# Kernel tuning notes

Hardware: AMD Instinct MI355X
Metric: run time of the kernel (lower is better)

## Reference

```python
import jax, jax.numpy as jnp
import numpy as np

N_NODES = 100000
N_EDGES = 6400000


def setup_inputs() -> dict:
    key = jax.random.key(0)
    ks = jax.random.split(key, 20)
    g = lambda i, shape, fan_in: jax.random.normal(ks[i], shape, dtype=jnp.float32) / np.sqrt(fan_in)
    inp = {
        "x": jax.random.normal(ks[0], (N_NODES, 32), dtype=jnp.float32),
        "edge_index": jax.random.randint(ks[1], (2, N_EDGES), 0, N_NODES, dtype=jnp.int64),
        # encoder: Linear(32,240) -> ReLU -> Linear(240,24) -> ReLU
        "enc_w1": g(2, (32, 240), 32), "enc_b1": jnp.zeros((240,), jnp.float32),
        "enc_w2": g(3, (240, 24), 240), "enc_b2": jnp.zeros((24,), jnp.float32),
        # lin_r (applied to root, no bias) -- PyG defaults
        "sage1_wl": g(4, (24, 24), 24), "sage1_bl": jnp.zeros((24,), jnp.float32), "sage1_wr": g(5, (24, 24), 24),
        "sage2_wl": g(6, (24, 24), 24), "sage2_bl": jnp.zeros((24,), jnp.float32), "sage2_wr": g(7, (24, 24), 24),
        "sage3_wl": g(8, (24, 24), 24), "sage3_bl": jnp.zeros((24,), jnp.float32), "sage3_wr": g(9, (24, 24), 24),
        # decoder: Linear(24,120) -> ReLU -> Linear(120,12)
        "dec_w1": g(10, (24, 120), 24), "dec_b1": jnp.zeros((120,), jnp.float32),
        "dec_w2": g(11, (120, 12), 120), "dec_b2": jnp.zeros((12,), jnp.float32),
    }
    return inp


def _sage_conv(x, src, dst, wl, bl, wr, n_nodes):
    # mean aggregation: gather source features, scatter-sum at targets, divide by degree
    msg = x[src]                                                   # [E, H]
    agg = jax.ops.segment_sum(msg, dst, num_segments=n_nodes)      # [N, H]
    deg = jax.ops.segment_sum(jnp.ones((src.shape[0],), x.dtype), dst, num_segments=n_nodes)
    mean = agg / jnp.maximum(deg, 1.0)[:, None]
    return mean @ wl + bl + x @ wr


def reference(x, edge_index, enc_w1, enc_b1, enc_w2, enc_b2,
              sage1_wl, sage1_bl, sage1_wr,
              sage2_wl, sage2_bl, sage2_wr,
              sage3_wl, sage3_bl, sage3_wr,
              dec_w1, dec_b1, dec_w2, dec_b2):
    n = x.shape[0]
    src, dst = edge_index[0], edge_index[1]
    # encoder
    h = jax.nn.relu(x @ enc_w1 + enc_b1)
    h = jax.nn.relu(h @ enc_w2 + enc_b2)
    # GNN: SAGEConv -> ReLU -> SAGEConv -> ReLU -> SAGEConv
    h = jax.nn.relu(_sage_conv(h, src, dst, sage1_wl, sage1_bl, sage1_wr, n))
    h = jax.nn.relu(_sage_conv(h, src, dst, sage2_wl, sage2_bl, sage2_wr, n))
    h = _sage_conv(h, src, dst, sage3_wl, sage3_bl, sage3_wr, n)
    # decoder
    h = jax.nn.relu(h @ dec_w1 + dec_b1)
    return h @ dec_w2 + dec_b2
```

## Files before the change

kernel.cpp:

```cpp
#include <hip/hip_runtime.h>
#include <hip/hip_bf16.h>

#define N_NODES 100000
#define N_EDGES 6400000
#define BROW 24
#define PROW 8
#define BUCKET_SIZE 256
#define N_BUCKETS ((N_NODES + BUCKET_SIZE - 1) / BUCKET_SIZE)
#define BUCKET_CAP 17408
#define STAGE_CAP 22528
#define SENT 0xFFFFFFFFu
#define STAGE_BLOCKS 512
#define CHUNK ((N_EDGES + STAGE_BLOCKS - 1) / STAGE_BLOCKS)

typedef float floatx2 __attribute__((ext_vector_type(2)));

__device__ __forceinline__ unsigned short f2bf(float f) {
    unsigned u = __float_as_uint(f);
    unsigned r = (u + 0x7fffu + ((u >> 16) & 1u)) >> 16;
    return (unsigned short)r;
}

__device__ __forceinline__ unsigned pack_fp8_4(float a, float b, float c, float d) {
    int w = __builtin_amdgcn_cvt_pk_fp8_f32(a, b, 0, false);
    w = __builtin_amdgcn_cvt_pk_fp8_f32(c, d, w, true);
    return (unsigned)w;
}

#define DEC4(w, arr, j) { \
    floatx2 lo_ = __builtin_amdgcn_cvt_pk_f32_fp8((int)(w), false); \
    floatx2 hi_ = __builtin_amdgcn_cvt_pk_f32_fp8((int)(w), true);  \
    arr[j] += lo_.x; arr[(j)+1] += lo_.y; arr[(j)+2] += hi_.x; arr[(j)+3] += hi_.y; }

#define SET2(u, arr, j) { arr[j] = __uint_as_float((u) << 16); arr[(j)+1] = __uint_as_float((u) & 0xffff0000u); }

__global__ __launch_bounds__(256) void k_transpose_w1(
    const float* __restrict__ w1, float* __restrict__ w1t)
{
    int tid = blockIdx.x * blockDim.x + threadIdx.x;
    if (tid < 32 * 240) {
        int k = tid >> 5, i = tid & 31;
        w1t[tid] = w1[i * 240 + k];
    }
}

__global__ __launch_bounds__(256) void k_enc_part(
    const float* __restrict__ x,
    const float* __restrict__ w1t, const float* __restrict__ b1,
    const float* __restrict__ w2,
    float* __restrict__ part)
{
    int nb = blockIdx.x >> 1;
    int chunk = blockIdx.x & 1;
    int n = nb * 256 + threadIdx.x;
    if (n >= N_NODES) return;

    float xr[32];
    const float4* xv = (const float4*)(x + (size_t)n * 32);
#pragma unroll
    for (int i = 0; i < 8; ++i) {
        float4 t = xv[i];
        xr[4*i+0] = t.x; xr[4*i+1] = t.y; xr[4*i+2] = t.z; xr[4*i+3] = t.w;
    }
    float acc[24];
#pragma unroll
    for (int j = 0; j < 24; ++j) acc[j] = 0.f;

    int k0 = chunk * 120;
    for (int k = k0; k < k0 + 120; ++k) {
        const float4* wr = (const float4*)(w1t + k * 32);
        float t = b1[k];
#pragma unroll
        for (int q = 0; q < 8; ++q) {
            float4 w = wr[q];
            t += xr[4*q+0] * w.x + xr[4*q+1] * w.y + xr[4*q+2] * w.z + xr[4*q+3] * w.w;
        }
        t = fmaxf(t, 0.f);
        const float* w2r = w2 + k * 24;
#pragma unroll
        for (int j = 0; j < 24; ++j) acc[j] += t * w2r[j];
    }
    float4* op = (float4*)(part + ((size_t)chunk * N_NODES + n) * 24);
#pragma unroll
    for (int c = 0; c < 6; ++c)
        op[c] = make_float4(acc[4*c], acc[4*c+1], acc[4*c+2], acc[4*c+3]);
}

__global__ __launch_bounds__(256) void k_enc_fin(
    const float* __restrict__ part, const float* __restrict__ b2,
    unsigned short* __restrict__ hb)
{
    int n = blockIdx.x * blockDim.x + threadIdx.x;
    if (n >= N_NODES) return;
    const float4* p0 = (const float4*)(part + (size_t)n * 24);
    const float4* p1 = (const float4*)(part + ((size_t)N_NODES + n) * 24);
    float acc[24];
#pragma unroll
    for (int c = 0; c < 6; ++c) {
        float4 a = p0[c], b = p1[c];
        acc[4*c+0] = a.x + b.x; acc[4*c+1] = a.y + b.y;
        acc[4*c+2] = a.z + b.z; acc[4*c+3] = a.w + b.w;
    }
    unsigned wb[12];
#pragma unroll
    for (int j = 0; j < 24; ++j) {
        float v = fmaxf(acc[j] + b2[j], 0.f);
        if (j & 1) wb[j >> 1] |= (unsigned)f2bf(v) << 16;
        else       wb[j >> 1]  = (unsigned)f2bf(v);
    }
    uint4* ob = (uint4*)(hb + (size_t)n * BROW);
#pragma unroll
    for (int q = 0; q < 3; ++q)
        ob[q] = make_uint4(wb[4*q], wb[4*q+1], wb[4*q+2], wb[4*q+3]);
}

__global__ __launch_bounds__(256) void k_stage1(
    const int* __restrict__ src, const int* __restrict__ dst,
    int* __restrict__ cursor, unsigned* __restrict__ stage)
{
    __shared__ int cnt[N_BUCKETS];
    __shared__ int bse[N_BUCKETS];
    __shared__ int lof[N_BUCKETS];
    __shared__ int cur[N_BUCKETS];
    __shared__ int ps[512];
    __shared__ unsigned sbuf[CHUNK];
    int t = threadIdx.x;
    int e0 = blockIdx.x * CHUNK;
    int e1 = min(e0 + CHUNK, N_EDGES);

    for (int i = t; i < N_BUCKETS; i += 256) cnt[i] = 0;
    __syncthreads();
    for (int e = e0 + t; e < e1; e += 256)
        atomicAdd(&cnt[dst[e] >> 8], 1);
    __syncthreads();
    for (int i = t; i < N_BUCKETS; i += 256) {
        int c = cnt[i];
        int c16 = (c + 15) & ~15;
        bse[i] = c16 ? atomicAdd(&cursor[i * 16], c16) : 0;
        cur[i] = 0;
    }
    ps[t]       = (t < N_BUCKETS) ? cnt[t] : 0;
    ps[t + 256] = (t + 256 < N_BUCKETS) ? cnt[t + 256] : 0;
    __syncthreads();
    for (int off = 1; off < 512; off <<= 1) {
        int a  = (t >= off) ? ps[t - off] : 0;
        int b2 = (t + 256 >= off) ? ps[t + 256 - off] : 0;
        __syncthreads();
        ps[t] += a;
        ps[t + 256] += b2;
        __syncthreads();
    }
    for (int i = t; i < N_BUCKETS; i += 256) lof[i] = ps[i] - cnt[i];
    __syncthreads();
    for (int e = e0 + t; e < e1; e += 256) {
        int d = dst[e];
        int s = src[e];
        int b = d >> 8;
        int pos = atomicAdd(&cur[b], 1);
        sbuf[lof[b] + pos] = ((unsigned)(d & 255) << 17) | (unsigned)s;
    }
    __syncthreads();
    int wid = t >> 6, lane = t & 63;
    for (int b = wid; b < N_BUCKETS; b += 4) {
        int c = cnt[b];
        int c16 = (c + 15) & ~15;
        unsigned* gp = stage + (size_t)b * STAGE_CAP + bse[b];
        const unsigned* lp = sbuf + lof[b];
        for (int j = lane; j < c16; j += 64)
            gp[j] = (j < c) ? lp[j] : SENT;
    }
}

__global__ __launch_bounds__(256) void k_fillcsr(
    const unsigned* __restrict__ stage, const int* __restrict__ cursor,
    int* __restrict__ csr, int* __restrict__ deg,
    float* __restrict__ recip, int* __restrict__ row_ptr)
{
    int b = blockIdx.x, t = threadIdx.x;
    __shared__ int dl[BUCKET_SIZE];
    __shared__ int s[BUCKET_SIZE];
    __shared__ int fcur[BUCKET_SIZE];
    int ne = cursor[b * 16];
    const unsigned* sp = stage + (size_t)b * STAGE_CAP;

    dl[t] = 0;
    __syncthreads();
    for (int i = t; i < ne; i += 256) {
        unsigned v = sp[i];
        if (v != SENT) atomicAdd(&dl[v >> 17], 1);
    }
    __syncthreads();
    int d = dl[t];
    s[t] = d;
    __syncthreads();
    for (int off = 1; off < 256; off <<= 1) {
        int v = (t >= off) ? s[t - off] : 0;
        __syncthreads();
        s[t] += v;
        __syncthreads();
    }
    int excl = s[t] - d;
    fcur[t] = excl;
    int n = b * BUCKET_SIZE + t;
    if (n < N_NODES) {
        deg[n] = d;
        recip[n] = 1.0f / (float)max(d, 1);
        row_ptr[n] = b * BUCKET_CAP + excl;
    }
    __syncthreads();
    int* cb = csr + (size_t)b * BUCKET_CAP;
    for (int i = t; i < ne; i += 256) {
        unsigned v = sp[i];
        if (v == SENT) continue;
        int slot = atomicAdd(&fcur[v >> 17], 1);
        cb[slot] = (int)(v & 0x1FFFFu);
    }
}

__global__ __launch_bounds__(256) void k_xform(
    const unsigned short* __restrict__ hin,
    const float* __restrict__ wl, const float* __restrict__ wr,
    unsigned* __restrict__ Ptab, float* __restrict__ Qtab)
{
    int n = blockIdx.x * blockDim.x + threadIdx.x;
    if (n >= N_NODES) return;
    float h[24];
    {
        const uint4* hp = (const uint4*)(hin + n * BROW);
        uint4 A = hp[0], B = hp[1], C = hp[2];
        SET2(A.x, h, 0)  SET2(A.y, h, 2)  SET2(A.z, h, 4)  SET2(A.w, h, 6)
        SET2(B.x, h, 8)  SET2(B.y, h,10)  SET2(B.z, h,12)  SET2(B.w, h,14)
        SET2(C.x, h,16)  SET2(C.y, h,18)  SET2(C.z, h,20)  SET2(C.w, h,22)
    }
    float p[24], q[24];
#pragma unroll
    for (int j = 0; j < 24; ++j) { p[j] = 0.f; q[j] = 0.f; }
#pragma unroll
    for (int k = 0; k < 24; ++k) {
        float hk = h[k];
#pragma unroll
        for (int j = 0; j < 24; ++j) {
            p[j] += hk * wl[k * 24 + j];
            q[j] += hk * wr[k * 24 + j];
        }
    }
    unsigned w8[6];
#pragma unroll
    for (int c = 0; c < 6; ++c)
        w8[c] = pack_fp8_4(p[4*c], p[4*c+1], p[4*c+2], p[4*c+3]);
    uint4* ob = (uint4*)(Ptab + (size_t)n * PROW);
    ob[0] = make_uint4(w8[0], w8[1], w8[2], w8[3]);
    ob[1] = make_uint4(w8[4], w8[5], 0u, 0u);
    float4* qb = (float4*)(Qtab + n * 24);
#pragma unroll
    for (int c = 0; c < 6; ++c)
        qb[c] = make_float4(q[4*c], q[4*c+1], q[4*c+2], q[4*c+3]);
}

template <bool RELU>
__global__ __launch_bounds__(256, 4) void k_agg(
    const unsigned* __restrict__ Ptab, const float* __restrict__ Qtab,
    const int* __restrict__ row_ptr, const int* __restrict__ deg,
    const float* __restrict__ recip, const int* __restrict__ csr,
    const float* __restrict__ bl,
    unsigned short* __restrict__ houtb)
{
    int gt = blockIdx.x * blockDim.x + threadIdx.x;
    int n = gt >> 3, g = gt & 7;
    if (n >= N_NODES) return;
    int start = row_ptr[n];
    int cnt = deg[n];

    float acc[24];
#pragma unroll
    for (int j = 0; j < 24; ++j) acc[j] = 0.f;

    for (int i = g; i < cnt; i += 8) {
        int s = __builtin_nontemporal_load(&csr[start + i]);
        const uint4* rp = (const uint4*)(Ptab + (size_t)s * PROW);
        uint4 A = rp[0];
        uint2 B = ((const uint2*)rp)[2];
        DEC4(A.x, acc, 0)  DEC4(A.y, acc, 4)  DEC4(A.z, acc, 8)
        DEC4(A.w, acc,12)  DEC4(B.x, acc,16)  DEC4(B.y, acc,20)
    }
#pragma unroll
    for (int m = 1; m <= 4; m <<= 1)
#pragma unroll
        for (int j = 0; j < 24; ++j) acc[j] += __shfl_xor(acc[j], m, 64);

    if (g < 3) {
        float rc = recip[n];
        const float4* qb = (const float4*)(Qtab + n * 24 + g * 8);
        float4 q0 = qb[0], q1 = qb[1];
        float qv[8] = {q0.x, q0.y, q0.z, q0.w, q1.x, q1.y, q1.z, q1.w};
        unsigned wb[4];
#pragma unroll
        for (int jj = 0; jj < 8; ++jj) {
            int j = g * 8 + jj;
            float v = acc[j] * rc + qv[jj] + bl[j];
            if (RELU) v = fmaxf(v, 0.f);
            if (jj & 1) wb[jj >> 1] |= (unsigned)f2bf(v) << 16;
            else        wb[jj >> 1]  = (unsigned)f2bf(v);
        }
        ((uint4*)(houtb + n * BROW))[g] = make_uint4(wb[0], wb[1], wb[2], wb[3]);
    }
}

__global__ __launch_bounds__(256, 4) void k_agg3(
    const unsigned* __restrict__ Ptab, const float* __restrict__ Qtab,
    const int* __restrict__ row_ptr, const int* __restrict__ deg,
    const float* __restrict__ recip, const int* __restrict__ csr,
    const float* __restrict__ bl,
    float* __restrict__ o3)
{
    int gt = blockIdx.x * blockDim.x + threadIdx.x;
    int n = gt >> 3, g = gt & 7;
    if (n >= N_NODES) return;
    int start = row_ptr[n];
    int cnt = deg[n];

    float acc[24];
#pragma unroll
    for (int j = 0; j < 24; ++j) acc[j] = 0.f;

    for (int i = g; i < cnt; i += 8) {
        int s = __builtin_nontemporal_load(&csr[start + i]);
        const uint4* rp = (const uint4*)(Ptab + (size_t)s * PROW);
        uint4 A = rp[0];
        uint2 B = ((const uint2*)rp)[2];
        DEC4(A.x, acc, 0)  DEC4(A.y, acc, 4)  DEC4(A.z, acc, 8)
        DEC4(A.w, acc,12)  DEC4(B.x, acc,16)  DEC4(B.y, acc,20)
    }
#pragma unroll
    for (int m = 1; m <= 4; m <<= 1)
#pragma unroll
        for (int j = 0; j < 24; ++j) acc[j] += __shfl_xor(acc[j], m, 64);

    if (g < 3) {
        float rc = recip[n];
        const float4* qb = (const float4*)(Qtab + n * 24 + g * 8);
        float4 q0 = qb[0], q1 = qb[1];
        float qv[8] = {q0.x, q0.y, q0.z, q0.w, q1.x, q1.y, q1.z, q1.w};
        float ov[8];
#pragma unroll
        for (int jj = 0; jj < 8; ++jj)
            ov[jj] = acc[g * 8 + jj] * rc + qv[jj] + bl[g * 8 + jj];
        float4* op = (float4*)(o3 + n * 24 + g * 8);
        op[0] = make_float4(ov[0], ov[1], ov[2], ov[3]);
        op[1] = make_float4(ov[4], ov[5], ov[6], ov[7]);
    }
}

__global__ __launch_bounds__(256) void k_decoder(
    const float* __restrict__ o3,
    const float* __restrict__ w1, const float* __restrict__ b1,
    const float* __restrict__ w2, const float* __restrict__ b2,
    float* __restrict__ out)
{
    int n = blockIdx.x * blockDim.x + threadIdx.x;
    if (n >= N_NODES) return;
    float h[24];
    const float4* hv = (const float4*)(o3 + (size_t)n * 24);
#pragma unroll
    for (int q = 0; q < 6; ++q) {
        float4 v = hv[q];
        h[4*q+0] = v.x; h[4*q+1] = v.y; h[4*q+2] = v.z; h[4*q+3] = v.w;
    }
    float acc[12];
#pragma unroll
    for (int j = 0; j < 12; ++j) acc[j] = b2[j];
    for (int k = 0; k < 120; ++k) {
        float t = b1[k];
#pragma unroll
        for (int i = 0; i < 24; ++i) t += h[i] * w1[i * 120 + k];
        t = fmaxf(t, 0.f);
#pragma unroll
        for (int j = 0; j < 12; ++j) acc[j] += t * w2[k * 12 + j];
    }
    float* o = out + (size_t)n * 12;
#pragma unroll
    for (int j = 0; j < 12; ++j) o[j] = acc[j];
}

static inline size_t align_up(size_t v, size_t a) { return (v + a - 1) & ~(a - 1); }

extern "C" void kernel_launch(void* const* d_in, const int* in_sizes, int n_in,
                              void* d_out, int out_size, void* d_ws, size_t ws_size,
                              hipStream_t stream)
{
    (void)in_sizes; (void)n_in; (void)out_size; (void)ws_size;

    const float* x    = (const float*)d_in[0];
    const int*  edge  = (const int*)d_in[1];
    const int*  esrc  = edge;
    const int*  edst  = edge + N_EDGES;
    const float* enc_w1 = (const float*)d_in[2];
    const float* enc_b1 = (const float*)d_in[3];
    const float* enc_w2 = (const float*)d_in[4];
    const float* enc_b2 = (const float*)d_in[5];
    const float* s1_wl = (const float*)d_in[6];
    const float* s1_bl = (const float*)d_in[7];
    const float* s1_wr = (const float*)d_in[8];
    const float* s2_wl = (const float*)d_in[9];
    const float* s2_bl = (const float*)d_in[10];
    const float* s2_wr = (const float*)d_in[11];
    const float* s3_wl = (const float*)d_in[12];
    const float* s3_bl = (const float*)d_in[13];
    const float* s3_wr = (const float*)d_in[14];
    const float* dec_w1 = (const float*)d_in[15];
    const float* dec_b1 = (const float*)d_in[16];
    const float* dec_w2 = (const float*)d_in[17];
    const float* dec_b2 = (const float*)d_in[18];
    float* out = (float*)d_out;

    char* base = (char*)d_ws;
    size_t off = 0;
    auto carve = [&](size_t bytes) { size_t o = off; off = align_up(off + bytes, 256); return (void*)(base + o); };
    char* stage_region = (char*)carve((size_t)N_BUCKETS * STAGE_CAP * sizeof(unsigned));
    unsigned* stage      = (unsigned*)stage_region;
    float* part          = (float*)stage_region;
    unsigned* Ptab       = (unsigned*)stage_region;
    float* Qtab          = (float*)(stage_region + 3200000);
    float* o3            = (float*)(stage_region + 12800000);
    int*   csr     = (int*)  carve((size_t)N_BUCKETS * BUCKET_CAP * sizeof(int));
    unsigned short* h0b = (unsigned short*)carve((size_t)N_NODES * BROW * sizeof(unsigned short));
    unsigned short* h1b = (unsigned short*)carve((size_t)N_NODES * BROW * sizeof(unsigned short));
    int*   deg     = (int*)  carve((size_t)N_NODES * sizeof(int));
    float* recip   = (float*)carve((size_t)N_NODES * sizeof(float));
    int*   row_ptr = (int*)  carve((size_t)N_NODES * sizeof(int));
    int*   cursor  = (int*)  carve((size_t)N_BUCKETS * 16 * sizeof(int));
    float* w1t     = (float*)carve((size_t)240 * 32 * sizeof(float));

    const int NB_N = (N_NODES + 255) / 256;
    const int NB8  = (N_NODES * 8 + 255) / 256;

    hipMemsetAsync(cursor, 0, (size_t)N_BUCKETS * 16 * sizeof(int), stream);
    k_stage1 <<<STAGE_BLOCKS, 256, 0, stream>>>(esrc, edst, cursor, stage);
    k_fillcsr<<<N_BUCKETS,   256, 0, stream>>>(stage, cursor, csr, deg, recip, row_ptr);

    k_transpose_w1<<<30, 256, 0, stream>>>(enc_w1, w1t);
    k_enc_part<<<NB_N * 2, 256, 0, stream>>>(x, w1t, enc_b1, enc_w2, part);
    k_enc_fin <<<NB_N,     256, 0, stream>>>(part, enc_b2, h0b);

    k_xform<<<NB_N, 256, 0, stream>>>(h0b, s1_wl, s1_wr, Ptab, Qtab);
    k_agg<true><<<NB8, 256, 0, stream>>>(Ptab, Qtab, row_ptr, deg, recip, csr, s1_bl, h1b);
    k_xform<<<NB_N, 256, 0, stream>>>(h1b, s2_wl, s2_wr, Ptab, Qtab);
    k_agg<true><<<NB8, 256, 0, stream>>>(Ptab, Qtab, row_ptr, deg, recip, csr, s2_bl, h0b);
    k_xform<<<NB_N, 256, 0, stream>>>(h0b, s3_wl, s3_wr, Ptab, Qtab);
    k_agg3<<<NB8, 256, 0, stream>>>(Ptab, Qtab, row_ptr, deg, recip, csr, s3_bl, o3);
    k_decoder<<<NB_N, 256, 0, stream>>>(o3, dec_w1, dec_b1, dec_w2, dec_b2, out);
}
```

Measured before the change: 527.5 us.

## Merge CSR fill with encoder into one launch and fuse encoder finish into xform

The CSR fill blocks and the encoder partial blocks now run in a single heterogeneous launch, so the graph-build work and the dense encoder can overlap on the device. The encoder partial sums are written as bf16 into the h0b/h1b buffers instead of fp32 into the stage region, which avoids overwriting stage before the fill reads it and halves the partial-sum traffic. The separate encoder-finish kernel is folded into the first xform, which now sums the two partials, adds the bias and applies ReLU before the SAGE transform. In exchange the partial sums are rounded to bf16 before they are added, which costs some precision, and the fused launch mixes block types with different resource needs.

Measured after the change: 484.5 us. -8.2%, faster.

```diff
diff --git a/kernel.cpp b/kernel.cpp
--- a/kernel.cpp
+++ b/kernel.cpp
@@ -33,6 +33,7 @@
     arr[j] += lo_.x; arr[(j)+1] += lo_.y; arr[(j)+2] += hi_.x; arr[(j)+3] += hi_.y; }
 
 #define SET2(u, arr, j) { arr[j] = __uint_as_float((u) << 16); arr[(j)+1] = __uint_as_float((u) & 0xffff0000u); }
+#define ADD2(u, arr, j) { arr[j] += __uint_as_float((u) << 16); arr[(j)+1] += __uint_as_float((u) & 0xffff0000u); }
 
 __global__ __launch_bounds__(256) void k_transpose_w1(
     const float* __restrict__ w1, float* __restrict__ w1t)
@@ -42,76 +43,6 @@
         int k = tid >> 5, i = tid & 31;
         w1t[tid] = w1[i * 240 + k];
     }
-}
-
-__global__ __launch_bounds__(256) void k_enc_part(
-    const float* __restrict__ x,
-    const float* __restrict__ w1t, const float* __restrict__ b1,
-    const float* __restrict__ w2,
-    float* __restrict__ part)
-{
-    int nb = blockIdx.x >> 1;
-    int chunk = blockIdx.x & 1;
-    int n = nb * 256 + threadIdx.x;
-    if (n >= N_NODES) return;
-
-    float xr[32];
-    const float4* xv = (const float4*)(x + (size_t)n * 32);
-#pragma unroll
-    for (int i = 0; i < 8; ++i) {
-        float4 t = xv[i];
-        xr[4*i+0] = t.x; xr[4*i+1] = t.y; xr[4*i+2] = t.z; xr[4*i+3] = t.w;
-    }
-    float acc[24];
-#pragma unroll
-    for (int j = 0; j < 24; ++j) acc[j] = 0.f;
-
-    int k0 = chunk * 120;
-    for (int k = k0; k < k0 + 120; ++k) {
-        const float4* wr = (const float4*)(w1t + k * 32);
-        float t = b1[k];
-#pragma unroll
-        for (int q = 0; q < 8; ++q) {
-            float4 w = wr[q];
-            t += xr[4*q+0] * w.x + xr[4*q+1] * w.y + xr[4*q+2] * w.z + xr[4*q+3] * w.w;
-        }
-        t = fmaxf(t, 0.f);
-        const float* w2r = w2 + k * 24;
-#pragma unroll
-        for (int j = 0; j < 24; ++j) acc[j] += t * w2r[j];
-    }
-    float4* op = (float4*)(part + ((size_t)chunk * N_NODES + n) * 24);
-#pragma unroll
-    for (int c = 0; c < 6; ++c)
-        op[c] = make_float4(acc[4*c], acc[4*c+1], acc[4*c+2], acc[4*c+3]);
-}
-
-__global__ __launch_bounds__(256) void k_enc_fin(
-    const float* __restrict__ part, const float* __restrict__ b2,
-    unsigned short* __restrict__ hb)
-{
-    int n = blockIdx.x * blockDim.x + threadIdx.x;
-    if (n >= N_NODES) return;
-    const float4* p0 = (const float4*)(part + (size_t)n * 24);
-    const float4* p1 = (const float4*)(part + ((size_t)N_NODES + n) * 24);
-    float acc[24];
-#pragma unroll
-    for (int c = 0; c < 6; ++c) {
-        float4 a = p0[c], b = p1[c];
-        acc[4*c+0] = a.x + b.x; acc[4*c+1] = a.y + b.y;
-        acc[4*c+2] = a.z + b.z; acc[4*c+3] = a.w + b.w;
-    }
-    unsigned wb[12];
-#pragma unroll
-    for (int j = 0; j < 24; ++j) {
-        float v = fmaxf(acc[j] + b2[j], 0.f);
-        if (j & 1) wb[j >> 1] |= (unsigned)f2bf(v) << 16;
-        else       wb[j >> 1]  = (unsigned)f2bf(v);
-    }
-    uint4* ob = (uint4*)(hb + (size_t)n * BROW);
-#pragma unroll
-    for (int q = 0; q < 3; ++q)
-        ob[q] = make_uint4(wb[4*q], wb[4*q+1], wb[4*q+2], wb[4*q+3]);
 }
 
 __global__ __launch_bounds__(256) void k_stage1(
@@ -171,50 +102,152 @@
     }
 }
 
-__global__ __launch_bounds__(256) void k_fillcsr(
+__global__ __launch_bounds__(256) void k_fill_enc(
     const unsigned* __restrict__ stage, const int* __restrict__ cursor,
     int* __restrict__ csr, int* __restrict__ deg,
-    float* __restrict__ recip, int* __restrict__ row_ptr)
-{
-    int b = blockIdx.x, t = threadIdx.x;
+    float* __restrict__ recip, int* __restrict__ row_ptr,
+    const float* __restrict__ x,
+    const float* __restrict__ w1t, const float* __restrict__ b1,
+    const float* __restrict__ w2,
+    unsigned short* __restrict__ pb0, unsigned short* __restrict__ pb1)
+{
     __shared__ int dl[BUCKET_SIZE];
     __shared__ int s[BUCKET_SIZE];
     __shared__ int fcur[BUCKET_SIZE];
-    int ne = cursor[b * 16];
-    const unsigned* sp = stage + (size_t)b * STAGE_CAP;
-
-    dl[t] = 0;
-    __syncthreads();
-    for (int i = t; i < ne; i += 256) {
-        unsigned v = sp[i];
-        if (v != SENT) atomicAdd(&dl[v >> 17], 1);
-    }
-    __syncthreads();
-    int d = dl[t];
-    s[t] = d;
-    __syncthreads();
-    for (int off = 1; off < 256; off <<= 1) {
-        int v = (t >= off) ? s[t - off] : 0;
-        __syncthreads();
-        s[t] += v;
-        __syncthreads();
-    }
-    int excl = s[t] - d;
-    fcur[t] = excl;
-    int n = b * BUCKET_SIZE + t;
-    if (n < N_NODES) {
-        deg[n] = d;
-        recip[n] = 1.0f / (float)max(d, 1);
-        row_ptr[n] = b * BUCKET_CAP + excl;
-    }
-    __syncthreads();
-    int* cb = csr + (size_t)b * BUCKET_CAP;
-    for (int i = t; i < ne; i += 256) {
-        unsigned v = sp[i];
-        if (v == SENT) continue;
-        int slot = atomicAdd(&fcur[v >> 17], 1);
-        cb[slot] = (int)(v & 0x1FFFFu);
-    }
+    int t = threadIdx.x;
+
+    if (blockIdx.x < N_BUCKETS) {
+        int b = blockIdx.x;
+        int ne = cursor[b * 16];
+        const unsigned* sp = stage + (size_t)b * STAGE_CAP;
+
+        dl[t] = 0;
+        __syncthreads();
+        for (int i = t; i < ne; i += 256) {
+            unsigned v = sp[i];
+            if (v != SENT) atomicAdd(&dl[v >> 17], 1);
+        }
+        __syncthreads();
+        int d = dl[t];
+        s[t] = d;
+        __syncthreads();
+        for (int off = 1; off < 256; off <<= 1) {
+            int v = (t >= off) ? s[t - off] : 0;
+            __syncthreads();
+            s[t] += v;
+            __syncthreads();
+        }
+        int excl = s[t] - d;
+        fcur[t] = excl;
+        int n = b * BUCKET_SIZE + t;
+        if (n < N_NODES) {
+            deg[n] = d;
+            recip[n] = 1.0f / (float)max(d, 1);
+            row_ptr[n] = b * BUCKET_CAP + excl;
+        }
+        __syncthreads();
+        int* cb = csr + (size_t)b * BUCKET_CAP;
+        for (int i = t; i < ne; i += 256) {
+            unsigned v = sp[i];
+            if (v == SENT) continue;
+            int slot = atomicAdd(&fcur[v >> 17], 1);
+            cb[slot] = (int)(v & 0x1FFFFu);
+        }
+    } else {
+        int bid = blockIdx.x - N_BUCKETS;
+        int nb = bid >> 1;
+        int chunk = bid & 1;
+        int n = nb * 256 + t;
+        if (n >= N_NODES) return;
+
+        float xr[32];
+        const float4* xv = (const float4*)(x + (size_t)n * 32);
+#pragma unroll
+        for (int i = 0; i < 8; ++i) {
+            float4 v = xv[i];
+            xr[4*i+0] = v.x; xr[4*i+1] = v.y; xr[4*i+2] = v.z; xr[4*i+3] = v.w;
+        }
+        float acc[24];
+#pragma unroll
+        for (int j = 0; j < 24; ++j) acc[j] = 0.f;
+
+        int k0 = chunk * 120;
+        for (int k = k0; k < k0 + 120; ++k) {
+            const float4* wr = (const float4*)(w1t + k * 32);
+            float tt = b1[k];
+#pragma unroll
+            for (int q = 0; q < 8; ++q) {
+                float4 w = wr[q];
+                tt += xr[4*q+0] * w.x + xr[4*q+1] * w.y + xr[4*q+2] * w.z + xr[4*q+3] * w.w;
+            }
+            tt = fmaxf(tt, 0.f);
+            const float* w2r = w2 + k * 24;
+#pragma unroll
+            for (int j = 0; j < 24; ++j) acc[j] += tt * w2r[j];
+        }
+        unsigned wb[12];
+#pragma unroll
+        for (int j = 0; j < 24; ++j) {
+            if (j & 1) wb[j >> 1] |= (unsigned)f2bf(acc[j]) << 16;
+            else       wb[j >> 1]  = (unsigned)f2bf(acc[j]);
+        }
+        unsigned short* pb = chunk ? pb1 : pb0;
+        uint4* ob = (uint4*)(pb + (size_t)n * BROW);
+#pragma unroll
+        for (int q = 0; q < 3; ++q)
+            ob[q] = make_uint4(wb[4*q], wb[4*q+1], wb[4*q+2], wb[4*q+3]);
+    }
+}
+
+__global__ __launch_bounds__(256) void k_encfin_xform(
+    const unsigned short* __restrict__ pb0, const unsigned short* __restrict__ pb1,
+    const float* __restrict__ b2,
+    const float* __restrict__ wl, const float* __restrict__ wr,
+    unsigned* __restrict__ Ptab, float* __restrict__ Qtab)
+{
+    int n = blockIdx.x * blockDim.x + threadIdx.x;
+    if (n >= N_NODES) return;
+    float h[24];
+    {
+        const uint4* hp = (const uint4*)(pb0 + (size_t)n * BROW);
+        uint4 A = hp[0], B = hp[1], C = hp[2];
+        SET2(A.x, h, 0)  SET2(A.y, h, 2)  SET2(A.z, h, 4)  SET2(A.w, h, 6)
+        SET2(B.x, h, 8)  SET2(B.y, h,10)  SET2(B.z, h,12)  SET2(B.w, h,14)
+        SET2(C.x, h,16)  SET2(C.y, h,18)  SET2(C.z, h,20)  SET2(C.w, h,22)
+    }
+    {
+        const uint4* hp = (const uint4*)(pb1 + (size_t)n * BROW);
+        uint4 A = hp[0], B = hp[1], C = hp[2];
+        ADD2(A.x, h, 0)  ADD2(A.y, h, 2)  ADD2(A.z, h, 4)  ADD2(A.w, h, 6)
+        ADD2(B.x, h, 8)  ADD2(B.y, h,10)  ADD2(B.z, h,12)  ADD2(B.w, h,14)
+        ADD2(C.x, h,16)  ADD2(C.y, h,18)  ADD2(C.z, h,20)  ADD2(C.w, h,22)
+    }
+#pragma unroll
+    for (int j = 0; j < 24; ++j) h[j] = fmaxf(h[j] + b2[j], 0.f);
+
+    float p[24], q[24];
+#pragma unroll
+    for (int j = 0; j < 24; ++j) { p[j] = 0.f; q[j] = 0.f; }
+#pragma unroll
+    for (int k = 0; k < 24; ++k) {
+        float hk = h[k];
+#pragma unroll
+        for (int j = 0; j < 24; ++j) {
+            p[j] += hk * wl[k * 24 + j];
+            q[j] += hk * wr[k * 24 + j];
+        }
+    }
+    unsigned w8[6];
+#pragma unroll
+    for (int c = 0; c < 6; ++c)
+        w8[c] = pack_fp8_4(p[4*c], p[4*c+1], p[4*c+2], p[4*c+3]);
+    uint4* ob = (uint4*)(Ptab + (size_t)n * PROW);
+    ob[0] = make_uint4(w8[0], w8[1], w8[2], w8[3]);
+    ob[1] = make_uint4(w8[4], w8[5], 0u, 0u);
+    float4* qb = (float4*)(Qtab + n * 24);
+#pragma unroll
+    for (int c = 0; c < 6; ++c)
+        qb[c] = make_float4(q[4*c], q[4*c+1], q[4*c+2], q[4*c+3]);
 }
 
 __global__ __launch_bounds__(256) void k_xform(
@@ -226,7 +259,7 @@
     if (n >= N_NODES) return;
     float h[24];
     {
-        const uint4* hp = (const uint4*)(hin + n * BROW);
+        const uint4* hp = (const uint4*)(hin + (size_t)n * BROW);
         uint4 A = hp[0], B = hp[1], C = hp[2];
         SET2(A.x, h, 0)  SET2(A.y, h, 2)  SET2(A.z, h, 4)  SET2(A.w, h, 6)
         SET2(B.x, h, 8)  SET2(B.y, h,10)  SET2(B.z, h,12)  SET2(B.w, h,14)
@@ -302,7 +335,7 @@
             if (jj & 1) wb[jj >> 1] |= (unsigned)f2bf(v) << 16;
             else        wb[jj >> 1]  = (unsigned)f2bf(v);
         }
-        ((uint4*)(houtb + n * BROW))[g] = make_uint4(wb[0], wb[1], wb[2], wb[3]);
+        ((uint4*)(houtb + (size_t)n * BROW))[g] = make_uint4(wb[0], wb[1], wb[2], wb[3]);
     }
 }
 
@@ -418,7 +451,6 @@
     auto carve = [&](size_t bytes) { size_t o = off; off = align_up(off + bytes, 256); return (void*)(base + o); };
     char* stage_region = (char*)carve((size_t)N_BUCKETS * STAGE_CAP * sizeof(unsigned));
     unsigned* stage      = (unsigned*)stage_region;
-    float* part          = (float*)stage_region;
     unsigned* Ptab       = (unsigned*)stage_region;
     float* Qtab          = (float*)(stage_region + 3200000);
     float* o3            = (float*)(stage_region + 12800000);
@@ -435,14 +467,14 @@
     const int NB8  = (N_NODES * 8 + 255) / 256;
 
     hipMemsetAsync(cursor, 0, (size_t)N_BUCKETS * 16 * sizeof(int), stream);
-    k_stage1 <<<STAGE_BLOCKS, 256, 0, stream>>>(esrc, edst, cursor, stage);
-    k_fillcsr<<<N_BUCKETS,   256, 0, stream>>>(stage, cursor, csr, deg, recip, row_ptr);
-
     k_transpose_w1<<<30, 256, 0, stream>>>(enc_w1, w1t);
-    k_enc_part<<<NB_N * 2, 256, 0, stream>>>(x, w1t, enc_b1, enc_w2, part);
-    k_enc_fin <<<NB_N,     256, 0, stream>>>(part, enc_b2, h0b);
-
-    k_xform<<<NB_N, 256, 0, stream>>>(h0b, s1_wl, s1_wr, Ptab, Qtab);
+    k_stage1<<<STAGE_BLOCKS, 256, 0, stream>>>(esrc, edst, cursor, stage);
+
+    k_fill_enc<<<NB_N + NB_N * 2, 256, 0, stream>>>(
+        stage, cursor, csr, deg, recip, row_ptr,
+        x, w1t, enc_b1, enc_w2, h0b, h1b);
+
+    k_encfin_xform<<<NB_N, 256, 0, stream>>>(h0b, h1b, enc_b2, s1_wl, s1_wr, Ptab, Qtab);
     k_agg<true><<<NB8, 256, 0, stream>>>(Ptab, Qtab, row_ptr, deg, recip, csr, s1_bl, h1b);
     k_xform<<<NB_N, 256, 0, stream>>>(h1b, s2_wl, s2_wr, Ptab, Qtab);
     k_agg<true><<<NB8, 256, 0, stream>>>(Ptab, Qtab, row_ptr, deg, recip, csr, s2_bl, h0b);
```
